# Kernel optimization log

Measured on AMD Instinct MI355X. Metric: run time of the kernel, lower is better.

## Reference

```python
import jax, jax.numpy as jnp
import numpy as np

D_MODEL = 1024
D_STATE = 16
D_CONV = 4
D_INNER = 2 * D_MODEL          # expand=2
DT_RANK = D_MODEL // 16        # math.ceil(1024/16) = 64
BATCH = 2
SEQ = 2048


def setup_inputs() -> dict:
    key = jax.random.key(0)
    ks = jax.random.split(key, 8)
    sc = lambda k, shape, s=0.02: jax.random.normal(k, shape, jnp.float32) * s
    x = jax.random.normal(ks[0], (BATCH, SEQ, D_MODEL), jnp.float32)
    in_proj_w = sc(ks[1], (2 * D_INNER, D_MODEL))
    conv_w = sc(ks[2], (D_INNER, 1, D_CONV), 0.2)   # depthwise causal conv kernel
    conv_b = jnp.zeros((D_INNER,), jnp.float32)
    x_proj_w = sc(ks[3], (DT_RANK + 2 * D_STATE, D_INNER))
    dt_proj_w = sc(ks[4], (D_INNER, DT_RANK), 0.1)
    # Mamba dt init: softplus^{-1}(dt) with dt ~ logUniform(1e-3, 0.1)
    dt = jnp.exp(jax.random.uniform(ks[5], (D_INNER,), jnp.float32)
                 * (np.log(0.1) - np.log(1e-3)) + np.log(1e-3))
    dt_proj_b = dt + jnp.log(-jnp.expm1(-dt))
    # A init: A[d, n] = n+1, stored as log
    A_log = jnp.log(jnp.tile(jnp.arange(1, D_STATE + 1, dtype=jnp.float32), (D_INNER, 1)))
    D = jnp.ones((D_INNER,), jnp.float32)
    out_proj_w = sc(ks[6], (D_MODEL, D_INNER))
    ln_g = jnp.ones((D_MODEL,), jnp.float32)
    ln_b = jnp.zeros((D_MODEL,), jnp.float32)
    return dict(x=x, ln_g=ln_g, ln_b=ln_b, in_proj_w=in_proj_w, conv_w=conv_w,
                conv_b=conv_b, x_proj_w=x_proj_w, dt_proj_w=dt_proj_w,
                dt_proj_b=dt_proj_b, A_log=A_log, D=D, out_proj_w=out_proj_w)


def reference(x, ln_g, ln_b, in_proj_w, conv_w, conv_b, x_proj_w,
              dt_proj_w, dt_proj_b, A_log, D, out_proj_w):
    # ---- LayerNorm (eps=1e-5, biased variance, matching torch) ----
    mu = jnp.mean(x, axis=-1, keepdims=True)
    var = jnp.mean((x - mu) ** 2, axis=-1, keepdims=True)
    xn = (x - mu) * jax.lax.rsqrt(var + 1e-5) * ln_g + ln_b

    # ---- Mamba: in_proj -> (x, z) ----
    xz = jnp.einsum('bld,ed->ble', xn, in_proj_w)        # (B, L, 2*D_INNER)
    xm, z = jnp.split(xz, 2, axis=-1)

    # ---- causal depthwise conv1d (kernel 4, left pad 3) + SiLU ----
    xc = jnp.transpose(xm, (0, 2, 1))                    # (B, D_INNER, L)
    xc = jax.lax.conv_general_dilated(
        xc, conv_w, window_strides=(1,), padding=[(D_CONV - 1, 0)],
        dimension_numbers=('NCH', 'OIH', 'NCH'),
        feature_group_count=D_INNER) + conv_b[None, :, None]
    xm = jax.nn.silu(jnp.transpose(xc, (0, 2, 1)))        # (B, L, D_INNER)

    # ---- SSM parameters per-timestep ----
    dbl = jnp.einsum('bld,ed->ble', xm, x_proj_w)         # (B, L, DT_RANK + 2*N)
    dt, Bs, Cs = jnp.split(dbl, [DT_RANK, DT_RANK + D_STATE], axis=-1)
    dt = jax.nn.softplus(jnp.einsum('blr,dr->bld', dt, dt_proj_w) + dt_proj_b)
    A = -jnp.exp(A_log)                                   # (D_INNER, N)

    # ---- selective scan over time ----
    def step(h, inp):
        dt_t, B_t, C_t, x_t = inp                         # (B,di),(B,N),(B,N),(B,di)
        dA = jnp.exp(dt_t[:, :, None] * A)                # (B, di, N)
        h = dA * h + (dt_t * x_t)[:, :, None] * B_t[:, None, :]
        y = jnp.einsum('bdn,bn->bd', h, C_t)
        return h, y

    h0 = jnp.zeros((x.shape[0], D_INNER, D_STATE), xm.dtype)
    inps = (jnp.transpose(dt, (1, 0, 2)), jnp.transpose(Bs, (1, 0, 2)),
            jnp.transpose(Cs, (1, 0, 2)), jnp.transpose(xm, (1, 0, 2)))
    _, ys = jax.lax.scan(step, h0, inps)                  # ys: (L, B, di)

    y = jnp.transpose(ys, (1, 0, 2)) + xm * D             # skip term D*x
    y = y * jax.nn.silu(z)                                # gate
    out = jnp.einsum('bld,ed->ble', y, out_proj_w)        # out_proj (no bias)
    return out + x                                        # residual
```

## Files before the change

### kernel.cpp

```cpp
#include <hip/hip_runtime.h>

typedef unsigned short u16;
typedef unsigned int u32;

#define LOG2E 1.44269504088896340736f

typedef __bf16 bf16x8 __attribute__((ext_vector_type(8)));
typedef float  f32x4  __attribute__((ext_vector_type(4)));
typedef u16    us8    __attribute__((ext_vector_type(8)));

__device__ __forceinline__ u16 f2bf(float f) {
  u32 u = __float_as_uint(f);
  u += 0x7FFF + ((u >> 16) & 1);
  return (u16)(u >> 16);
}
__device__ __forceinline__ float bf2f(u16 h) {
  return __uint_as_float(((u32)h) << 16);
}

template <int CTRL>
__device__ __forceinline__ float dppadd(float p) {
  return p + __uint_as_float(__builtin_amdgcn_update_dpp(
      0u, __float_as_uint(p), CTRL, 0xF, 0xF, true));
}

__device__ __forceinline__ void gload_lds16(const u16* g, u16* l) {
  __builtin_amdgcn_global_load_lds(
      (const __attribute__((address_space(1))) u16*)g,
      (__attribute__((address_space(3))) u16*)l, 16, 0, 0);
}

__global__ __launch_bounds__(256) void cvt_all(
    const float* __restrict__ s0, u16* __restrict__ d0, int n0,
    const float* __restrict__ s1, u16* __restrict__ d1, int n1,
    const float* __restrict__ s2, u16* __restrict__ d2, int n2,
    const float* __restrict__ s3, u16* __restrict__ d3, int n3) {
  int i = (blockIdx.x * 256 + threadIdx.x) * 8;
  const float* s; u16* d;
  if (i < n0) { s = s0; d = d0; }
  else {
    i -= n0;
    if (i < n1) { s = s1; d = d1; }
    else {
      i -= n1;
      if (i < n2) { s = s2; d = d2; }
      else { i -= n2; if (i >= n3) return; s = s3; d = d3; }
    }
  }
  float4 a = *(const float4*)(s + i);
  float4 b = *(const float4*)(s + i + 4);
  us8 o;
  o[0] = f2bf(a.x); o[1] = f2bf(a.y); o[2] = f2bf(a.z); o[3] = f2bf(a.w);
  o[4] = f2bf(b.x); o[5] = f2bf(b.y); o[6] = f2bf(b.z); o[7] = f2bf(b.w);
  *(us8*)(d + i) = o;
}

__global__ __launch_bounds__(256) void ln_kernel(const float* __restrict__ x,
                                                 const float* __restrict__ g,
                                                 const float* __restrict__ b,
                                                 u16* __restrict__ xn) {
  int row = blockIdx.x;
  int tid = threadIdx.x;
  const float4 v = ((const float4*)(x + (size_t)row * 1024))[tid];
  float s  = v.x + v.y + v.z + v.w;
  float s2 = v.x * v.x + v.y * v.y + v.z * v.z + v.w * v.w;
  __shared__ float r0[256], r1[256];
  r0[tid] = s; r1[tid] = s2;
  __syncthreads();
  for (int off = 128; off > 0; off >>= 1) {
    if (tid < off) { r0[tid] += r0[tid + off]; r1[tid] += r1[tid + off]; }
    __syncthreads();
  }
  float mu  = r0[0] * (1.f / 1024.f);
  float var = r1[0] * (1.f / 1024.f) - mu * mu;
  float inv = rsqrtf(var + 1e-5f);
  float4 gg = ((const float4*)g)[tid];
  float4 bb = ((const float4*)b)[tid];
  ushort4 o;
  o.x = f2bf((v.x - mu) * inv * gg.x + bb.x);
  o.y = f2bf((v.y - mu) * inv * gg.y + bb.y);
  o.z = f2bf((v.z - mu) * inv * gg.z + bb.z);
  o.w = f2bf((v.w - mu) * inv * gg.w + bb.w);
  ((ushort4*)(xn + (size_t)row * 1024))[tid] = o;
}

template <int EPI>
__global__ __launch_bounds__(256, 2) void gemm_lds(const u16* __restrict__ A,
                                                   const u16* __restrict__ W,
                                                   int M, int N, int K,
                                                   u16* __restrict__ outb,
                                                   float* __restrict__ outf,
                                                   const float* __restrict__ res) {
  __shared__ u16 As[128 * 64];
  __shared__ u16 Ws[128 * 64];
  int tid = threadIdx.x;
  int wid = tid >> 6, lane = tid & 63;
  int wm = wid >> 1, wn = wid & 1;
  int nwg = (gridDim.x * gridDim.y);
  int orig = blockIdx.y * gridDim.x + blockIdx.x;
  int q = nwg >> 3;
  int swz = (orig & 7) * q + (orig >> 3);
  int bx = swz & 31;
  int by = swz >> 5;
  int m0 = bx * 128, n0 = by * 128;
  int srow = lane >> 3, scol = (lane & 7) * 8;
  int lr = lane & 15, lk8 = (lane >> 4) * 8;
  f32x4 acc[4][4] = {};

  for (int k = 0; k < K; k += 64) {
    __syncthreads();
#pragma unroll
    for (int i = 0; i < 4; ++i) {
      int chunk = wid * 4 + i;
      int row = chunk * 8 + srow;
      gload_lds16(A + (size_t)(m0 + row) * K + k + scol, As + chunk * 512);
      gload_lds16(W + (size_t)(n0 + row) * K + k + scol, Ws + chunk * 512);
    }
    __syncthreads();
#pragma unroll
    for (int kk = 0; kk < 2; ++kk) {
      bf16x8 af[4], wf[4];
#pragma unroll
      for (int i = 0; i < 4; ++i) {
        af[i] = *(const bf16x8*)(As + (wm * 64 + i * 16 + lr) * 64 + kk * 32 + lk8);
        wf[i] = *(const bf16x8*)(Ws + (wn * 64 + i * 16 + lr) * 64 + kk * 32 + lk8);
      }
#pragma unroll
      for (int i = 0; i < 4; ++i)
#pragma unroll
        for (int j = 0; j < 4; ++j)
          acc[i][j] = __builtin_amdgcn_mfma_f32_16x16x32_bf16(af[i], wf[j], acc[i][j], 0, 0, 0);
    }
  }

  int cr = (lane >> 4) * 4;
#pragma unroll
  for (int i = 0; i < 4; ++i) {
#pragma unroll
    for (int j = 0; j < 4; ++j) {
      int col = n0 + wn * 64 + j * 16 + lr;
#pragma unroll
      for (int r = 0; r < 4; ++r) {
        int row = m0 + wm * 64 + i * 16 + cr + r;
        float v = acc[i][j][r];
        if (EPI == 0) outb[(size_t)row * N + col] = f2bf(v);
        else          outf[(size_t)row * N + col] = v + res[(size_t)row * N + col];
      }
    }
  }
}

__global__ __launch_bounds__(256) void gemm_dt(const u16* __restrict__ A,
                                               const u16* __restrict__ W,
                                               int M, int N, int K,
                                               u16* __restrict__ outb,
                                               const float* __restrict__ bias) {
  int wid = threadIdx.x >> 6;
  int lane = threadIdx.x & 63;
  int wm = wid >> 1, wn = wid & 1;
  int m0 = blockIdx.x * 128 + wm * 64;
  int n0 = blockIdx.y * 128 + wn * 64;
  int lr = lane & 15;
  int lk = (lane >> 4) * 8;
  f32x4 acc[4][4] = {};
  for (int k = 0; k < K; k += 32) {
    bf16x8 af[4], bfr[4];
#pragma unroll
    for (int i = 0; i < 4; i++)
      af[i] = *(const bf16x8*)(A + (size_t)(m0 + i * 16 + lr) * K + k + lk);
#pragma unroll
    for (int j = 0; j < 4; j++)
      bfr[j] = *(const bf16x8*)(W + (size_t)(n0 + j * 16 + lr) * K + k + lk);
#pragma unroll
    for (int i = 0; i < 4; i++)
#pragma unroll
      for (int j = 0; j < 4; j++)
        acc[i][j] = __builtin_amdgcn_mfma_f32_16x16x32_bf16(af[i], bfr[j], acc[i][j], 0, 0, 0);
  }
  int cr = (lane >> 4) * 4;
#pragma unroll
  for (int i = 0; i < 4; i++) {
#pragma unroll
    for (int j = 0; j < 4; j++) {
      int col = n0 + j * 16 + lr;
#pragma unroll
      for (int r = 0; r < 4; r++) {
        int row = m0 + i * 16 + cr + r;
        float v = acc[i][j][r] + bias[row];
        v = (v > 15.f) ? v : log1pf(__expf(v));
        outb[(size_t)row * N + col] = f2bf(v);
      }
    }
  }
}

__global__ __launch_bounds__(256) void gemm_xproj(const u16* __restrict__ A,
                                                  const u16* __restrict__ W,
                                                  u16* __restrict__ dtr,
                                                  float* __restrict__ bc,
                                                  int M, int K) {
  __shared__ float red[4][96][16];
  int tid = threadIdx.x;
  int wid = tid >> 6, lane = tid & 63;
  int m0 = blockIdx.x * 16;
  int kq = K >> 2;
  int k0 = wid * kq;
  int lr = lane & 15;
  int lk = (lane >> 4) * 8;
  f32x4 acc[6] = {};
  for (int k = k0; k < k0 + kq; k += 32) {
    bf16x8 af = *(const bf16x8*)(A + (size_t)(m0 + lr) * K + k + lk);
#pragma unroll
    for (int j = 0; j < 6; j++) {
      bf16x8 bfr = *(const bf16x8*)(W + (size_t)(j * 16 + lr) * K + k + lk);
      acc[j] = __builtin_amdgcn_mfma_f32_16x16x32_bf16(af, bfr, acc[j], 0, 0, 0);
    }
  }
  int cr = (lane >> 4) * 4;
#pragma unroll
  for (int j = 0; j < 6; j++)
#pragma unroll
    for (int r = 0; r < 4; r++)
      red[wid][j * 16 + lr][cr + r] = acc[j][r];
  __syncthreads();
#pragma unroll
  for (int o = tid; o < 1536; o += 256) {
    int col = o >> 4, r16 = o & 15;
    float s = red[0][col][r16] + red[1][col][r16] + red[2][col][r16] + red[3][col][r16];
    int row = m0 + r16;
    if (col < 64) dtr[(size_t)row * 64 + col] = f2bf(s);
    else          bc[(size_t)row * 32 + (col - 64)] = s;
  }
}

__global__ __launch_bounds__(256) void conv_tr(const u16* __restrict__ xz,
                                               const float* __restrict__ cw,
                                               const float* __restrict__ cb,
                                               u16* __restrict__ xm,
                                               u16* __restrict__ xmT) {
  __shared__ u16 xin[67 * 72];
  __shared__ u16 xout[64 * 72];
  __shared__ float4 cwl[64];
  __shared__ float cbl[64];
  int tid = threadIdx.x;
  int d0 = blockIdx.x * 64, t0 = blockIdx.y * 64, b = blockIdx.z;
  if (tid < 64) {
    cwl[tid] = *(const float4*)(cw + (d0 + tid) * 4);
    cbl[tid] = cb[d0 + tid];
  }
  for (int task = tid; task < 536; task += 256) {
    int r = task >> 3, c8 = (task & 7) * 8;
    int t = t0 - 3 + r;
    us8 v = {0, 0, 0, 0, 0, 0, 0, 0};
    if (t >= 0) v = *(const us8*)(xz + (size_t)(b * 2048 + t) * 4096 + d0 + c8);
    *(us8*)(xin + r * 72 + c8) = v;
  }
  __syncthreads();
  for (int task = tid; task < 512; task += 256) {
    int tr = task >> 3, c8 = (task & 7) * 8;
    us8 a0 = *(const us8*)(xin + tr * 72 + c8);
    us8 a1 = *(const us8*)(xin + (tr + 1) * 72 + c8);
    us8 a2 = *(const us8*)(xin + (tr + 2) * 72 + c8);
    us8 a3 = *(const us8*)(xin + (tr + 3) * 72 + c8);
    us8 o;
#pragma unroll
    for (int j = 0; j < 8; ++j) {
      float4 w = cwl[c8 + j];
      float acc = cbl[c8 + j] + w.x * bf2f(a0[j]) + w.y * bf2f(a1[j])
                + w.z * bf2f(a2[j]) + w.w * bf2f(a3[j]);
      float s = acc / (1.f + __expf(-acc));
      o[j] = f2bf(s);
      xout[(c8 + j) * 72 + tr] = o[j];
    }
    *(us8*)(xm + (size_t)(b * 2048 + t0 + tr) * 2048 + d0 + c8) = o;
  }
  __syncthreads();
  for (int task = tid; task < 512; task += 256) {
    int dl = task >> 3, t8 = (task & 7) * 8;
    us8 v = *(const us8*)(xout + dl * 72 + t8);
    *(us8*)(xmT + (size_t)(d0 + dl) * 4096 + b * 2048 + t0 + t8) = v;
  }
}

__global__ __launch_bounds__(256, 4) void scan_pass1(
    const u16* __restrict__ dtT, const u16* __restrict__ xmT,
    const float* __restrict__ bc, const float* __restrict__ A_log,
    float* __restrict__ Pbuf, float* __restrict__ Sbuf) {
  __shared__ float bcs[64 * 32];
  int tid = threadIdx.x;
  int chunk = blockIdx.y;
  int chan = blockIdx.x * 64 + (tid >> 2);
  int n0 = (tid & 3) * 4;
  int b = chan >> 11, d = chan & 2047;
  int t0 = chunk * 64;
  {
    const float4* src = (const float4*)(bc + (size_t)(b * 2048 + t0) * 32);
    ((float4*)bcs)[tid] = src[tid];
    ((float4*)bcs)[tid + 256] = src[tid + 256];
  }
  float a2[4];
#pragma unroll
  for (int i = 0; i < 4; ++i)
    a2[i] = -__expf(A_log[d * 16 + n0 + i]) * LOG2E;
  __syncthreads();
  const us8* dtp = (const us8*)(dtT + (size_t)d * 4096 + b * 2048 + t0);
  const us8* xmp = (const us8*)(xmT + (size_t)d * 4096 + b * 2048 + t0);
  float h[4] = {};
  float sdt = 0.f;
  for (int blk = 0; blk < 8; ++blk) {
    us8 dt8 = dtp[blk], xm8 = xmp[blk];
#pragma unroll
    for (int j = 0; j < 8; ++j) {
      float dtv = bf2f(dt8[j]);
      float dtx = dtv * bf2f(xm8[j]);
      sdt += dtv;
      f32x4 Bv = *(const f32x4*)(bcs + (blk * 8 + j) * 32 + n0);
#pragma unroll
      for (int i = 0; i < 4; ++i) {
        float dA = exp2f(dtv * a2[i]);
        h[i] = dA * h[i] + dtx * Bv[i];
      }
    }
  }
  size_t oidx = (size_t)chunk * 65536 + (size_t)chan * 16 + n0;
  f32x4 P;
#pragma unroll
  for (int i = 0; i < 4; ++i) P[i] = exp2f(sdt * a2[i]);
  *(f32x4*)(Pbuf + oidx) = P;
  *(f32x4*)(Sbuf + oidx) = *(f32x4*)h;
}

__global__ __launch_bounds__(256) void scan_carry(const float* __restrict__ Pbuf,
                                                  const float* __restrict__ Sbuf,
                                                  float* __restrict__ Hin) {
  int idx = blockIdx.x * 256 + threadIdx.x;
  float h = 0.f;
  Hin[idx] = 0.f;
  for (int c = 1; c < 32; ++c) {
    h = Pbuf[(size_t)(c - 1) * 65536 + idx] * h + Sbuf[(size_t)(c - 1) * 65536 + idx];
    Hin[(size_t)c * 65536 + idx] = h;
  }
}

__global__ __launch_bounds__(256, 4) void scan_pass2(
    const u16* __restrict__ dtT, const u16* __restrict__ xmT,
    const float* __restrict__ bc, const u16* __restrict__ xz,
    const float* __restrict__ A_log, const float* __restrict__ Dp,
    const float* __restrict__ Hin, u16* __restrict__ yg) {
  __shared__ float bcs[64 * 32];
  int tid = threadIdx.x;
  int chunk = blockIdx.y;
  int chan = blockIdx.x * 64 + (tid >> 2);
  int n0 = (tid & 3) * 4;
  int b = chan >> 11, d = chan & 2047;
  int t0 = chunk * 64;
  {
    const float4* src = (const float4*)(bc + (size_t)(b * 2048 + t0) * 32);
    ((float4*)bcs)[tid] = src[tid];
    ((float4*)bcs)[tid + 256] = src[tid + 256];
  }
  float a2[4];
#pragma unroll
  for (int i = 0; i < 4; ++i)
    a2[i] = -__expf(A_log[d * 16 + n0 + i]) * LOG2E;
  __syncthreads();
  const us8* dtp = (const us8*)(dtT + (size_t)d * 4096 + b * 2048 + t0);
  const us8* xmp = (const us8*)(xmT + (size_t)d * 4096 + b * 2048 + t0);
  float Dd = Dp[d];
  f32x4 hv = *(const f32x4*)(Hin + (size_t)chunk * 65536 + (size_t)chan * 16 + n0);
  float h0 = hv[0], h1 = hv[1], h2 = hv[2], h3 = hv[3];
  bool leader = (tid & 3) == 0;
  for (int blk = 0; blk < 8; ++blk) {
    us8 dt8 = dtp[blk], xm8 = xmp[blk];
    u16 z8[8];
#pragma unroll
    for (int j = 0; j < 8; ++j)
      z8[j] = xz[(size_t)(b * 2048 + t0 + blk * 8 + j) * 4096 + 2048 + d];
#pragma unroll
    for (int j = 0; j < 8; ++j) {
      int tl = blk * 8 + j;
      float dtv = bf2f(dt8[j]);
      float xv  = bf2f(xm8[j]);
      float dtx = dtv * xv;
      f32x4 Bv = *(const f32x4*)(bcs + tl * 32 + n0);
      f32x4 Cv = *(const f32x4*)(bcs + tl * 32 + 16 + n0);
      float dA0 = exp2f(dtv * a2[0]);
      float dA1 = exp2f(dtv * a2[1]);
      float dA2 = exp2f(dtv * a2[2]);
      float dA3 = exp2f(dtv * a2[3]);
      h0 = dA0 * h0 + dtx * Bv[0];
      h1 = dA1 * h1 + dtx * Bv[1];
      h2 = dA2 * h2 + dtx * Bv[2];
      h3 = dA3 * h3 + dtx * Bv[3];
      float p = (h0 * Cv[0] + h2 * Cv[2]) + (h1 * Cv[1] + h3 * Cv[3]);
      p = dppadd<0xB1>(p);
      p = dppadd<0x4E>(p);
      float zf = bf2f(z8[j]);
      float g = zf / (1.f + __expf(-zf));
      float yv = (p + Dd * xv) * g;
      if (leader)
        yg[(size_t)(b * 2048 + t0 + tl) * 2048 + d] = f2bf(yv);
    }
  }
}

extern "C" void kernel_launch(void* const* d_in, const int* in_sizes, int n_in,
                              void* d_out, int out_size, void* d_ws, size_t ws_size,
                              hipStream_t stream) {
  const float* x         = (const float*)d_in[0];
  const float* ln_g      = (const float*)d_in[1];
  const float* ln_b      = (const float*)d_in[2];
  const float* in_proj_w = (const float*)d_in[3];
  const float* conv_w    = (const float*)d_in[4];
  const float* conv_b    = (const float*)d_in[5];
  const float* x_proj_w  = (const float*)d_in[6];
  const float* dt_proj_w = (const float*)d_in[7];
  const float* dt_proj_b = (const float*)d_in[8];
  const float* A_log     = (const float*)d_in[9];
  const float* Dp        = (const float*)d_in[10];
  const float* out_proj_w= (const float*)d_in[11];
  float* out = (float*)d_out;

  const int B = 2, L = 2048, DM = 1024, DI = 2048;
  const int M = B * L;

  char* ws = (char*)d_ws;
  size_t off = 0;
  auto alloc = [&](size_t bytes) {
    void* p = ws + off;
    off += (bytes + 255) & ~(size_t)255;
    return p;
  };
  u16*   yg    = (u16*)ws;
  u16*   xn    = (u16*)alloc((size_t)M * DM * 2);
  u16*   w_in  = (u16*)alloc((size_t)2 * DI * DM * 2);
  u16*   w_out = (u16*)alloc((size_t)DM * DI * 2);
  u16*   w_x   = (u16*)alloc((size_t)96 * DI * 2);
  u16*   w_dt  = (u16*)alloc((size_t)DI * 64 * 2);
  u16*   xz    = (u16*)alloc((size_t)M * 2 * DI * 2);
  u16*   bufA  = (u16*)alloc((size_t)M * DI * 2);
  u16*   bufB  = (u16*)alloc((size_t)M * DI * 2);
  u16*   dtr   = (u16*)alloc((size_t)M * 64 * 2);
  float* bc    = (float*)alloc((size_t)M * 32 * 4);
  float* Pbuf  = (float*)alloc((size_t)31 * 65536 * 4);
  float* Sbuf  = (float*)alloc((size_t)31 * 65536 * 4);
  float* Hin   = (float*)alloc((size_t)32 * 65536 * 4);

  u16* xm  = bufA;
  u16* dtT = bufA;
  u16* xmT = bufB;

  cvt_all<<<3280, 256, 0, stream>>>(in_proj_w, w_in, 2 * DI * DM,
                                    out_proj_w, w_out, DM * DI,
                                    x_proj_w, w_x, 96 * DI,
                                    dt_proj_w, w_dt, DI * 64);

  ln_kernel<<<M, 256, 0, stream>>>(x, ln_g, ln_b, xn);

  gemm_lds<0><<<dim3(M / 128, (2 * DI) / 128), 256, 0, stream>>>(
      xn, w_in, M, 2 * DI, DM, xz, nullptr, nullptr);

  conv_tr<<<dim3(DI / 64, L / 64, B), 256, 0, stream>>>(xz, conv_w, conv_b, xm, xmT);

  gemm_xproj<<<M / 16, 256, 0, stream>>>(xm, w_x, dtr, bc, M, DI);

  gemm_dt<<<dim3(DI / 128, M / 128), 256, 0, stream>>>(
      w_dt, dtr, DI, M, 64, dtT, dt_proj_b);

  scan_pass1<<<dim3(M / 64, 31), 256, 0, stream>>>(dtT, xmT, bc, A_log, Pbuf, Sbuf);
  scan_carry<<<256, 256, 0, stream>>>(Pbuf, Sbuf, Hin);
  scan_pass2<<<dim3(M / 64, 32), 256, 0, stream>>>(dtT, xmT, bc, xz, A_log, Dp, Hin, yg);

  gemm_lds<2><<<dim3(M / 128, DM / 128), 256, 0, stream>>>(
      yg, w_out, M, DM, DI, nullptr, out, x);
}
```

Baseline: 312.5 us.

## Double-buffer GEMM k-tiles, fold scan carry into pass2, spread gate epilogue across lanes

The LDS GEMM now uses two 32-wide k buffers and prefetches the next tile while the current one runs through MFMA, which drops one barrier per iteration. The separate scan_carry kernel and its Hin buffer are removed. Each scan_pass2 block instead recomputes its incoming state by walking the earlier chunks' P/S values, which saves a launch and a round trip through global memory but adds up to 31 serial steps for late chunks. The pass2 epilogue is also restructured so that all four lanes of a channel group share the z loads, SiLU gating and y stores instead of one leader lane doing them.

Result: faster. 281.7 us (-9.9%).

```diff
diff --git a/kernel.cpp b/kernel.cpp
--- a/kernel.cpp
+++ b/kernel.cpp
@@ -91,8 +91,8 @@
                                                    u16* __restrict__ outb,
                                                    float* __restrict__ outf,
                                                    const float* __restrict__ res) {
-  __shared__ u16 As[128 * 64];
-  __shared__ u16 Ws[128 * 64];
+  __shared__ u16 As[2][128 * 32];
+  __shared__ u16 Ws[2][128 * 32];
   int tid = threadIdx.x;
   int wid = tid >> 6, lane = tid & 63;
   int wm = wid >> 1, wn = wid & 1;
@@ -103,34 +103,43 @@
   int bx = swz & 31;
   int by = swz >> 5;
   int m0 = bx * 128, n0 = by * 128;
-  int srow = lane >> 3, scol = (lane & 7) * 8;
+  int srow = lane >> 2, skel = (lane & 3) * 8;
   int lr = lane & 15, lk8 = (lane >> 4) * 8;
   f32x4 acc[4][4] = {};
-
-  for (int k = 0; k < K; k += 64) {
+  int nt = K >> 5;
+
+#pragma unroll
+  for (int i = 0; i < 2; ++i) {
+    int chunk = wid * 2 + i;
+    int row = chunk * 16 + srow;
+    gload_lds16(A + (size_t)(m0 + row) * K + skel, As[0] + chunk * 512);
+    gload_lds16(W + (size_t)(n0 + row) * K + skel, Ws[0] + chunk * 512);
+  }
+
+  for (int kt = 0; kt < nt; ++kt) {
     __syncthreads();
+    int cur = kt & 1;
+    if (kt + 1 < nt) {
+      int k = (kt + 1) << 5;
+#pragma unroll
+      for (int i = 0; i < 2; ++i) {
+        int chunk = wid * 2 + i;
+        int row = chunk * 16 + srow;
+        gload_lds16(A + (size_t)(m0 + row) * K + k + skel, As[cur ^ 1] + chunk * 512);
+        gload_lds16(W + (size_t)(n0 + row) * K + k + skel, Ws[cur ^ 1] + chunk * 512);
+      }
+    }
+    bf16x8 af[4], wf[4];
 #pragma unroll
     for (int i = 0; i < 4; ++i) {
-      int chunk = wid * 4 + i;
-      int row = chunk * 8 + srow;
-      gload_lds16(A + (size_t)(m0 + row) * K + k + scol, As + chunk * 512);
-      gload_lds16(W + (size_t)(n0 + row) * K + k + scol, Ws + chunk * 512);
-    }
-    __syncthreads();
-#pragma unroll
-    for (int kk = 0; kk < 2; ++kk) {
-      bf16x8 af[4], wf[4];
-#pragma unroll
-      for (int i = 0; i < 4; ++i) {
-        af[i] = *(const bf16x8*)(As + (wm * 64 + i * 16 + lr) * 64 + kk * 32 + lk8);
-        wf[i] = *(const bf16x8*)(Ws + (wn * 64 + i * 16 + lr) * 64 + kk * 32 + lk8);
-      }
-#pragma unroll
-      for (int i = 0; i < 4; ++i)
-#pragma unroll
-        for (int j = 0; j < 4; ++j)
-          acc[i][j] = __builtin_amdgcn_mfma_f32_16x16x32_bf16(af[i], wf[j], acc[i][j], 0, 0, 0);
-    }
+      af[i] = *(const bf16x8*)(As[cur] + (wm * 64 + i * 16 + lr) * 32 + lk8);
+      wf[i] = *(const bf16x8*)(Ws[cur] + (wn * 64 + i * 16 + lr) * 32 + lk8);
+    }
+#pragma unroll
+    for (int i = 0; i < 4; ++i)
+#pragma unroll
+      for (int j = 0; j < 4; ++j)
+        acc[i][j] = __builtin_amdgcn_mfma_f32_16x16x32_bf16(af[i], wf[j], acc[i][j], 0, 0, 0);
   }
 
   int cr = (lane >> 4) * 4;
@@ -330,28 +339,18 @@
   *(f32x4*)(Sbuf + oidx) = *(f32x4*)h;
 }
 
-__global__ __launch_bounds__(256) void scan_carry(const float* __restrict__ Pbuf,
-                                                  const float* __restrict__ Sbuf,
-                                                  float* __restrict__ Hin) {
-  int idx = blockIdx.x * 256 + threadIdx.x;
-  float h = 0.f;
-  Hin[idx] = 0.f;
-  for (int c = 1; c < 32; ++c) {
-    h = Pbuf[(size_t)(c - 1) * 65536 + idx] * h + Sbuf[(size_t)(c - 1) * 65536 + idx];
-    Hin[(size_t)c * 65536 + idx] = h;
-  }
-}
-
 __global__ __launch_bounds__(256, 4) void scan_pass2(
     const u16* __restrict__ dtT, const u16* __restrict__ xmT,
     const float* __restrict__ bc, const u16* __restrict__ xz,
     const float* __restrict__ A_log, const float* __restrict__ Dp,
-    const float* __restrict__ Hin, u16* __restrict__ yg) {
+    const float* __restrict__ Pbuf, const float* __restrict__ Sbuf,
+    u16* __restrict__ yg) {
   __shared__ float bcs[64 * 32];
   int tid = threadIdx.x;
   int chunk = blockIdx.y;
   int chan = blockIdx.x * 64 + (tid >> 2);
-  int n0 = (tid & 3) * 4;
+  int m = tid & 3;
+  int n0 = m * 4;
   int b = chan >> 11, d = chan & 2047;
   int t0 = chunk * 64;
   {
@@ -363,44 +362,60 @@
 #pragma unroll
   for (int i = 0; i < 4; ++i)
     a2[i] = -__expf(A_log[d * 16 + n0 + i]) * LOG2E;
+
+  f32x4 hv = {0.f, 0.f, 0.f, 0.f};
+  {
+    size_t cidx = (size_t)chan * 16 + n0;
+#pragma unroll 2
+    for (int c = 0; c < chunk; ++c) {
+      f32x4 P = *(const f32x4*)(Pbuf + (size_t)c * 65536 + cidx);
+      f32x4 S = *(const f32x4*)(Sbuf + (size_t)c * 65536 + cidx);
+#pragma unroll
+      for (int i = 0; i < 4; ++i) hv[i] = P[i] * hv[i] + S[i];
+    }
+  }
   __syncthreads();
   const us8* dtp = (const us8*)(dtT + (size_t)d * 4096 + b * 2048 + t0);
   const us8* xmp = (const us8*)(xmT + (size_t)d * 4096 + b * 2048 + t0);
   float Dd = Dp[d];
-  f32x4 hv = *(const f32x4*)(Hin + (size_t)chunk * 65536 + (size_t)chan * 16 + n0);
   float h0 = hv[0], h1 = hv[1], h2 = hv[2], h3 = hv[3];
-  bool leader = (tid & 3) == 0;
+  bool s0 = (m & 1) != 0, s1 = (m & 2) != 0;
+  int ja = 2 * m, jb = 2 * m + 1;
+  size_t zrow = (size_t)(b * 2048 + t0) * 4096 + 2048 + d;
+  size_t yrow = (size_t)(b * 2048 + t0) * 2048 + d;
   for (int blk = 0; blk < 8; ++blk) {
     us8 dt8 = dtp[blk], xm8 = xmp[blk];
-    u16 z8[8];
-#pragma unroll
-    for (int j = 0; j < 8; ++j)
-      z8[j] = xz[(size_t)(b * 2048 + t0 + blk * 8 + j) * 4096 + 2048 + d];
+    float p[8], xv[8];
 #pragma unroll
     for (int j = 0; j < 8; ++j) {
       int tl = blk * 8 + j;
       float dtv = bf2f(dt8[j]);
-      float xv  = bf2f(xm8[j]);
-      float dtx = dtv * xv;
+      xv[j] = bf2f(xm8[j]);
+      float dtx = dtv * xv[j];
       f32x4 Bv = *(const f32x4*)(bcs + tl * 32 + n0);
       f32x4 Cv = *(const f32x4*)(bcs + tl * 32 + 16 + n0);
-      float dA0 = exp2f(dtv * a2[0]);
-      float dA1 = exp2f(dtv * a2[1]);
-      float dA2 = exp2f(dtv * a2[2]);
-      float dA3 = exp2f(dtv * a2[3]);
-      h0 = dA0 * h0 + dtx * Bv[0];
-      h1 = dA1 * h1 + dtx * Bv[1];
-      h2 = dA2 * h2 + dtx * Bv[2];
-      h3 = dA3 * h3 + dtx * Bv[3];
-      float p = (h0 * Cv[0] + h2 * Cv[2]) + (h1 * Cv[1] + h3 * Cv[3]);
-      p = dppadd<0xB1>(p);
-      p = dppadd<0x4E>(p);
-      float zf = bf2f(z8[j]);
-      float g = zf / (1.f + __expf(-zf));
-      float yv = (p + Dd * xv) * g;
-      if (leader)
-        yg[(size_t)(b * 2048 + t0 + tl) * 2048 + d] = f2bf(yv);
-    }
+      h0 = exp2f(dtv * a2[0]) * h0 + dtx * Bv[0];
+      h1 = exp2f(dtv * a2[1]) * h1 + dtx * Bv[1];
+      h2 = exp2f(dtv * a2[2]) * h2 + dtx * Bv[2];
+      h3 = exp2f(dtv * a2[3]) * h3 + dtx * Bv[3];
+      p[j] = (h0 * Cv[0] + h2 * Cv[2]) + (h1 * Cv[1] + h3 * Cv[3]);
+    }
+#pragma unroll
+    for (int j = 0; j < 8; ++j) p[j] = dppadd<0xB1>(p[j]);
+#pragma unroll
+    for (int j = 0; j < 8; ++j) p[j] = dppadd<0x4E>(p[j]);
+    float pa = s1 ? (s0 ? p[6] : p[4]) : (s0 ? p[2] : p[0]);
+    float pb = s1 ? (s0 ? p[7] : p[5]) : (s0 ? p[3] : p[1]);
+    float xa = s1 ? (s0 ? xv[6] : xv[4]) : (s0 ? xv[2] : xv[0]);
+    float xb = s1 ? (s0 ? xv[7] : xv[5]) : (s0 ? xv[3] : xv[1]);
+    float za = bf2f(xz[zrow + (size_t)(blk * 8 + ja) * 4096]);
+    float zb = bf2f(xz[zrow + (size_t)(blk * 8 + jb) * 4096]);
+    float ga = za / (1.f + __expf(-za));
+    float gb = zb / (1.f + __expf(-zb));
+    float ya = (pa + Dd * xa) * ga;
+    float yb = (pb + Dd * xb) * gb;
+    yg[yrow + (size_t)(blk * 8 + ja) * 2048] = f2bf(ya);
+    yg[yrow + (size_t)(blk * 8 + jb) * 2048] = f2bf(yb);
   }
 }
 
@@ -444,7 +459,6 @@
   float* bc    = (float*)alloc((size_t)M * 32 * 4);
   float* Pbuf  = (float*)alloc((size_t)31 * 65536 * 4);
   float* Sbuf  = (float*)alloc((size_t)31 * 65536 * 4);
-  float* Hin   = (float*)alloc((size_t)32 * 65536 * 4);
 
   u16* xm  = bufA;
   u16* dtT = bufA;
@@ -468,8 +482,8 @@
       w_dt, dtr, DI, M, 64, dtT, dt_proj_b);
 
   scan_pass1<<<dim3(M / 64, 31), 256, 0, stream>>>(dtT, xmT, bc, A_log, Pbuf, Sbuf);
-  scan_carry<<<256, 256, 0, stream>>>(Pbuf, Sbuf, Hin);
-  scan_pass2<<<dim3(M / 64, 32), 256, 0, stream>>>(dtT, xmT, bc, xz, A_log, Dp, Hin, yg);
+  scan_pass2<<<dim3(M / 64, 32), 256, 0, stream>>>(dtT, xmT, bc, xz, A_log, Dp,
+                                                   Pbuf, Sbuf, yg);
 
   gemm_lds<2><<<dim3(M / 128, DM / 128), 256, 0, stream>>>(
       yg, w_out, M, DM, DI, nullptr, out, x);
```
